# Kernel tuning notes

Hardware: AMD Instinct MI355X
Metric: run time of the kernel (lower is better)

The kernel has to match this reference:

```python
import jax, jax.numpy as jnp
import numpy as np

B, C, H, W = 4, 256, 64, 64
C8 = C // 8


def setup_inputs() -> dict:
    key = jax.random.key(0)
    k1, k2, k3, k4 = jax.random.split(key, 4)
    x = jax.random.normal(k1, (B, C, H, W), dtype=jnp.float32)
    # conv1d(ks=1, bias=False) projections -> plain [out, in] matrices
    Wq = jax.random.normal(k2, (C8, C), dtype=jnp.float32) * (1.0 / np.sqrt(C))
    Wk = jax.random.normal(k3, (C8, C), dtype=jnp.float32) * (1.0 / np.sqrt(C))
    Wv = jax.random.normal(k4, (C, C), dtype=jnp.float32) * (1.0 / np.sqrt(C))
    gamma = jnp.zeros((1,), dtype=jnp.float32)
    return {"x": x, "Wq": Wq, "Wk": Wk, "Wv": Wv, "gamma": gamma}


def reference(x, Wq, Wk, Wv, gamma):
    b, c, h, w = x.shape
    xf = x.reshape(b, c, h * w)                      # [B, C, N]
    f = jnp.einsum('oc,bcn->bon', Wq, xf)            # [B, C/8, N] query
    g = jnp.einsum('oc,bcn->bon', Wk, xf)            # [B, C/8, N] key
    hv = jnp.einsum('oc,bcn->bon', Wv, xf)           # [B, C,   N] value
    # scores[b,i,j] = sum_c f[b,c,i] * g[b,c,j]; softmax over dim=1 (i)
    scores = jnp.einsum('bci,bcj->bij', f, g)        # [B, N, N]
    beta = jax.nn.softmax(scores, axis=1)
    # o[b,c,j] = sum_i hv[b,c,i] * beta[b,i,j]
    o = jnp.einsum('bci,bij->bcj', hv, beta)         # [B, C, N]
    out = gamma[0] * o + xf
    return out.reshape(b, c, h, w)
```

## Files before the change

kernel.cpp:

```cpp
#include <hip/hip_runtime.h>

#define B_  4
#define C_  256
#define C8_ 32
#define N_  4096

#define TJ 128
#define KI 64
#define SPLITS 4

typedef __attribute__((ext_vector_type(8)))  short bf16x8;
typedef __attribute__((ext_vector_type(16))) float f32x16;

union FragAB { bf16x8 v; unsigned short u[8]; };

__device__ __forceinline__ unsigned short f2bf(float x) {
    unsigned u = __float_as_uint(x);
    unsigned r = u + 0x7FFFu + ((u >> 16) & 1u);
    return (unsigned short)(r >> 16);
}
__device__ __forceinline__ unsigned pack2bf(float a, float b) {
    return (unsigned)f2bf(a) | ((unsigned)f2bf(b) << 16);
}

__global__ __launch_bounds__(256) void prep_w_kernel(
    const float* __restrict__ Wq, const float* __restrict__ Wk,
    const float* __restrict__ Wv, unsigned short* __restrict__ Wbf)
{
    int idx = (blockIdx.x * 256 + threadIdx.x) * 4;
    int row = idx >> 8;
    int col = idx & 255;
    const float* src; int r;
    if (row < 32)      { src = Wq; r = row;      }
    else if (row < 64) { src = Wk; r = row - 32; }
    else               { src = Wv; r = row - 64; }
    float4 v = *(const float4*)&src[r * 256 + col];
    uint2 o; o.x = pack2bf(v.x, v.y); o.y = pack2bf(v.z, v.w);
    *(uint2*)&Wbf[idx] = o;
}

__global__ __launch_bounds__(256) void prep_x_kernel(
    const float* __restrict__ x, unsigned short* __restrict__ xT)
{
    __shared__ unsigned short T[64][66];
    int t  = threadIdx.x;
    int b  = blockIdx.z;
    int c0 = blockIdx.y * 64;
    int n0 = blockIdx.x * 64;
    const float* xb = x + (size_t)b * C_ * N_;
    int n_l = t & 63, c_l = t >> 6;
#pragma unroll
    for (int q = 0; q < 16; ++q) {
        int c = c_l * 16 + q;
        T[n_l][c] = f2bf(xb[(size_t)(c0 + c) * N_ + n0 + n_l]);
    }
    __syncthreads();
    unsigned short* xTb = xT + (size_t)b * N_ * C_;
    int c_l2 = t & 63, nb = t >> 6;
#pragma unroll
    for (int q = 0; q < 16; ++q) {
        int n = nb * 16 + q;
        xTb[(size_t)(n0 + n) * C_ + c0 + c_l2] = T[n][c_l2];
    }
}

__global__ __launch_bounds__(256) void proj_mfma_kernel(
    const unsigned short* __restrict__ Wbf, const unsigned short* __restrict__ xT,
    unsigned short* __restrict__ f, unsigned short* __restrict__ g,
    unsigned short* __restrict__ hv)
{
    int t = threadIdx.x, w = t >> 6, lane = t & 63;
    int half = lane >> 5, l31 = lane & 31;
    int b  = blockIdx.y;
    int n0 = blockIdx.x * 32;

    const unsigned short* xb = xT + ((size_t)b * N_ + n0 + l31) * C_;
    int nm = (w < 2) ? 3 : 2;
    int mt0 = w, mt1 = w + 4, mt2 = w + 8;

    f32x16 acc[3];
#pragma unroll
    for (int a = 0; a < 3; ++a) acc[a] = (f32x16)0.f;

#pragma unroll
    for (int ks = 0; ks < 16; ++ks) {
        int kofs = ks * 16 + half * 8;
        bf16x8 bfr = *(const bf16x8*)&xb[kofs];
        bf16x8 a0 = *(const bf16x8*)&Wbf[(size_t)(mt0 * 32 + l31) * 256 + kofs];
        acc[0] = __builtin_amdgcn_mfma_f32_32x32x16_bf16(a0, bfr, acc[0], 0, 0, 0);
        bf16x8 a1 = *(const bf16x8*)&Wbf[(size_t)(mt1 * 32 + l31) * 256 + kofs];
        acc[1] = __builtin_amdgcn_mfma_f32_32x32x16_bf16(a1, bfr, acc[1], 0, 0, 0);
        if (nm == 3) {
            bf16x8 a2 = *(const bf16x8*)&Wbf[(size_t)(mt2 * 32 + l31) * 256 + kofs];
            acc[2] = __builtin_amdgcn_mfma_f32_32x32x16_bf16(a2, bfr, acc[2], 0, 0, 0);
        }
    }

    unsigned short* fb = f  + (size_t)b * C8_ * N_;
    unsigned short* gb = g  + (size_t)b * C8_ * N_;
    unsigned short* hb = hv + (size_t)b * C_  * N_;
#pragma unroll
    for (int im = 0; im < 3; ++im) {
        if (im >= nm) break;
        int mt = (im == 0) ? mt0 : (im == 1) ? mt1 : mt2;
#pragma unroll
        for (int r = 0; r < 16; ++r) {
            int R = mt * 32 + (r & 3) + 8 * (r >> 2) + 4 * half;
            unsigned short v = f2bf(acc[im][r]);
            if (R < 32)       fb[(size_t)R * N_ + n0 + l31] = v;
            else if (R < 64)  gb[(size_t)(R - 64 + 32) * N_ + n0 + l31] = v;
            else              hb[(size_t)(R - 64) * N_ + n0 + l31] = v;
        }
    }
}

__global__ __launch_bounds__(256, 2) void flash_kernel(
    const unsigned short* __restrict__ f, const unsigned short* __restrict__ g,
    const unsigned short* __restrict__ hv, float* __restrict__ o_part,
    float* __restrict__ l_part)
{
    __shared__ unsigned short fT[64][40];
    __shared__ unsigned short hvT[256][72];
    __shared__ unsigned short pT[128][72];

    int t    = threadIdx.x;
    int w    = t >> 6;
    int lane = t & 63;
    int half = lane >> 5;
    int l31  = lane & 31;

    int b  = blockIdx.z;
    int s  = blockIdx.y;
    int j0 = blockIdx.x * TJ;

    const unsigned short* fb = f  + (size_t)b * C8_ * N_;
    const unsigned short* gb = g  + (size_t)b * C8_ * N_;
    const unsigned short* hb = hv + (size_t)b * C_  * N_;

    FragAB gf[2];
#pragma unroll
    for (int ks = 0; ks < 2; ++ks)
#pragma unroll
        for (int r = 0; r < 8; ++r) {
            int ch = ks * 16 + half * 8 + r;
            gf[ks].u[r] = gb[(size_t)ch * N_ + j0 + w * 32 + l31];
        }

    f32x16 acc[8];
#pragma unroll
    for (int a = 0; a < 8; ++a) acc[a] = (f32x16)0.f;
    float lacc = 0.f;

    int i_begin = s * (N_ / SPLITS);
    int i_end   = i_begin + N_ / SPLITS;

    for (int i0 = i_begin; i0 < i_end; i0 += KI) {
        __syncthreads();

        {
            int i   = t & 63;
            int chb = (t >> 6) * 8;
            unsigned short v[8];
#pragma unroll
            for (int q = 0; q < 8; ++q)
                v[q] = fb[(size_t)(chb + q) * N_ + i0 + i];
#pragma unroll
            for (int q = 0; q < 4; ++q)
                *(unsigned*)&fT[i][chb + 2 * q] =
                    (unsigned)v[2 * q] | ((unsigned)v[2 * q + 1] << 16);
        }
        {
            int crow  = t >> 3;
            int chunk = t & 7;
#pragma unroll
            for (int q = 0; q < 8; ++q) {
                int c = crow + 32 * q;
                uint4 v = *(const uint4*)&hb[(size_t)c * N_ + i0 + chunk * 8];
                *(uint4*)&hvT[c][chunk * 8] = v;
            }
        }
        __syncthreads();

#pragma unroll
        for (int it = 0; it < 2; ++it) {
            f32x16 sacc = (f32x16)0.f;
#pragma unroll
            for (int ks = 0; ks < 2; ++ks) {
                bf16x8 af = *(const bf16x8*)&fT[it * 32 + l31][ks * 16 + half * 8];
                sacc = __builtin_amdgcn_mfma_f32_32x32x16_bf16(af, gf[ks].v, sacc, 0, 0, 0);
            }
            float p[16];
#pragma unroll
            for (int r = 0; r < 16; ++r) {
                p[r] = __expf(sacc[r]);
                lacc += p[r];
            }
            int jr = w * 32 + l31;
#pragma unroll
            for (int a = 0; a < 4; ++a) {
                unsigned u0 = pack2bf(p[4 * a + 0], p[4 * a + 1]);
                unsigned u1 = pack2bf(p[4 * a + 2], p[4 * a + 3]);
                uint2 v; v.x = u0; v.y = u1;
                *(uint2*)&pT[jr][it * 32 + 8 * a + 4 * half] = v;
            }
        }
        __syncthreads();

#pragma unroll
        for (int ks4 = 0; ks4 < 4; ++ks4) {
            int kofs = ks4 * 16 + half * 8;
            bf16x8 af[2], bfr[4];
#pragma unroll
            for (int ct = 0; ct < 2; ++ct)
                af[ct] = *(const bf16x8*)&hvT[w * 64 + ct * 32 + l31][kofs];
#pragma unroll
            for (int jt = 0; jt < 4; ++jt)
                bfr[jt] = *(const bf16x8*)&pT[jt * 32 + l31][kofs];
#pragma unroll
            for (int ct = 0; ct < 2; ++ct)
#pragma unroll
                for (int jt = 0; jt < 4; ++jt)
                    acc[ct * 4 + jt] = __builtin_amdgcn_mfma_f32_32x32x16_bf16(
                        af[ct], bfr[jt], acc[ct * 4 + jt], 0, 0, 0);
        }
    }

    float* ob = o_part + (size_t)(b * SPLITS + s) * C_ * N_;
#pragma unroll
    for (int ct = 0; ct < 2; ++ct)
#pragma unroll
        for (int jt = 0; jt < 4; ++jt) {
            f32x16 a = acc[ct * 4 + jt];
#pragma unroll
            for (int r = 0; r < 16; ++r) {
                int c = w * 64 + ct * 32 + (r & 3) + 8 * (r >> 2) + 4 * half;
                int j = j0 + jt * 32 + l31;
                ob[(size_t)c * N_ + j] = a[r];
            }
        }
    float lsum = lacc + __shfl_down(lacc, 32);
    if (lane < 32)
        l_part[(size_t)(b * SPLITS + s) * N_ + j0 + w * 32 + lane] = lsum;
}

__global__ __launch_bounds__(256) void combine_kernel(
    const float* __restrict__ o_part, const float* __restrict__ l_part,
    const float* __restrict__ x, const float* __restrict__ gamma,
    float* __restrict__ out)
{
    int j = blockIdx.x * 256 + threadIdx.x;
    int b = blockIdx.z;
    float l = 0.f;
#pragma unroll
    for (int s = 0; s < SPLITS; ++s)
        l += l_part[(size_t)(b * SPLITS + s) * N_ + j];
    float inv = 1.f / l;
    float gm = gamma[0];
#pragma unroll
    for (int cc = 0; cc < 4; ++cc) {
        int c = blockIdx.y * 4 + cc;
        float o = 0.f;
#pragma unroll
        for (int s = 0; s < SPLITS; ++s)
            o += o_part[((size_t)(b * SPLITS + s) * C_ + c) * N_ + j];
        size_t idx = ((size_t)b * C_ + c) * N_ + j;
        out[idx] = gm * o * inv + x[idx];
    }
}

extern "C" void kernel_launch(void* const* d_in, const int* in_sizes, int n_in,
                              void* d_out, int out_size, void* d_ws, size_t ws_size,
                              hipStream_t stream) {
    const float* x     = (const float*)d_in[0];
    const float* Wq    = (const float*)d_in[1];
    const float* Wk    = (const float*)d_in[2];
    const float* Wv    = (const float*)d_in[3];
    const float* gamma = (const float*)d_in[4];
    float* out = (float*)d_out;

    char* ws = (char*)d_ws;
    float* o_part = (float*)ws;
    float* l_part = o_part + (size_t)SPLITS * B_ * C_ * N_;
    unsigned short* f   = (unsigned short*)(l_part + (size_t)SPLITS * B_ * N_);
    unsigned short* g   = f   + (size_t)B_ * C8_ * N_;
    unsigned short* hv  = g   + (size_t)B_ * C8_ * N_;
    unsigned short* Wbf = hv  + (size_t)B_ * C_  * N_;
    unsigned short* xT  = Wbf + (size_t)(C_ + 2 * C8_) * C_;

    prep_w_kernel<<<dim3(80), 256, 0, stream>>>(Wq, Wk, Wv, Wbf);
    prep_x_kernel<<<dim3(N_ / 64, C_ / 64, B_), 256, 0, stream>>>(x, xT);

    proj_mfma_kernel<<<dim3(N_ / 32, B_), 256, 0, stream>>>(Wbf, xT, f, g, hv);

    flash_kernel<<<dim3(N_ / TJ, SPLITS, B_), 256, 0, stream>>>(f, g, hv, o_part, l_part);

    combine_kernel<<<dim3(N_ / 256, C_ / 4, B_), 256, 0, stream>>>(o_part, l_part, x, gamma, out);
}
```

Baseline: 158.8 us.

## Split flash kernel over channel halves, read operands directly from global, bf16 partials

```diff
diff --git a/kernel.cpp b/kernel.cpp
--- a/kernel.cpp
+++ b/kernel.cpp
@@ -21,6 +21,9 @@
 }
 __device__ __forceinline__ unsigned pack2bf(float a, float b) {
     return (unsigned)f2bf(a) | ((unsigned)f2bf(b) << 16);
+}
+__device__ __forceinline__ float bf2f(unsigned short h) {
+    return __uint_as_float(((unsigned)h) << 16);
 }
 
 __global__ __launch_bounds__(256) void prep_w_kernel(
@@ -66,7 +69,7 @@
 
 __global__ __launch_bounds__(256) void proj_mfma_kernel(
     const unsigned short* __restrict__ Wbf, const unsigned short* __restrict__ xT,
-    unsigned short* __restrict__ f, unsigned short* __restrict__ g,
+    unsigned short* __restrict__ fTg, unsigned short* __restrict__ g,
     unsigned short* __restrict__ hv)
 {
     int t = threadIdx.x, w = t >> 6, lane = t & 63;
@@ -96,7 +99,6 @@
         }
     }
 
-    unsigned short* fb = f  + (size_t)b * C8_ * N_;
     unsigned short* gb = g  + (size_t)b * C8_ * N_;
     unsigned short* hb = hv + (size_t)b * C_  * N_;
 #pragma unroll
@@ -107,21 +109,19 @@
         for (int r = 0; r < 16; ++r) {
             int R = mt * 32 + (r & 3) + 8 * (r >> 2) + 4 * half;
             unsigned short v = f2bf(acc[im][r]);
-            if (R < 32)       fb[(size_t)R * N_ + n0 + l31] = v;
-            else if (R < 64)  gb[(size_t)(R - 64 + 32) * N_ + n0 + l31] = v;
+            if (R < 32)       fTg[((size_t)b * N_ + n0 + l31) * 32 + R] = v;
+            else if (R < 64)  gb[(size_t)(R - 32) * N_ + n0 + l31] = v;
             else              hb[(size_t)(R - 64) * N_ + n0 + l31] = v;
         }
     }
 }
 
-__global__ __launch_bounds__(256, 2) void flash_kernel(
-    const unsigned short* __restrict__ f, const unsigned short* __restrict__ g,
-    const unsigned short* __restrict__ hv, float* __restrict__ o_part,
+__global__ __launch_bounds__(256, 3) void flash_kernel(
+    const unsigned short* __restrict__ fTg, const unsigned short* __restrict__ g,
+    const unsigned short* __restrict__ hv, unsigned short* __restrict__ o_part,
     float* __restrict__ l_part)
 {
-    __shared__ unsigned short fT[64][40];
-    __shared__ unsigned short hvT[256][72];
-    __shared__ unsigned short pT[128][72];
+    __shared__ unsigned short pT[2][128][72];
 
     int t    = threadIdx.x;
     int w    = t >> 6;
@@ -129,13 +129,15 @@
     int half = lane >> 5;
     int l31  = lane & 31;
 
-    int b  = blockIdx.z;
-    int s  = blockIdx.y;
-    int j0 = blockIdx.x * TJ;
-
-    const unsigned short* fb = f  + (size_t)b * C8_ * N_;
-    const unsigned short* gb = g  + (size_t)b * C8_ * N_;
-    const unsigned short* hb = hv + (size_t)b * C_  * N_;
+    int j0    = blockIdx.x * TJ;
+    int chalf = blockIdx.y;
+    int bs    = blockIdx.z;
+    int b     = bs >> 2;
+    int s     = bs & 3;
+
+    const unsigned short* fb = fTg + (size_t)b * N_ * 32;
+    const unsigned short* gb = g   + (size_t)b * C8_ * N_;
+    const unsigned short* hrow = hv + ((size_t)b * C_ + chalf * 128 + w * 32 + l31) * N_;
 
     FragAB gf[2];
 #pragma unroll
@@ -146,47 +148,24 @@
             gf[ks].u[r] = gb[(size_t)ch * N_ + j0 + w * 32 + l31];
         }
 
-    f32x16 acc[8];
-#pragma unroll
-    for (int a = 0; a < 8; ++a) acc[a] = (f32x16)0.f;
+    f32x16 acc[4];
+#pragma unroll
+    for (int a = 0; a < 4; ++a) acc[a] = (f32x16)0.f;
     float lacc = 0.f;
 
     int i_begin = s * (N_ / SPLITS);
-    int i_end   = i_begin + N_ / SPLITS;
-
-    for (int i0 = i_begin; i0 < i_end; i0 += KI) {
-        __syncthreads();
-
-        {
-            int i   = t & 63;
-            int chb = (t >> 6) * 8;
-            unsigned short v[8];
-#pragma unroll
-            for (int q = 0; q < 8; ++q)
-                v[q] = fb[(size_t)(chb + q) * N_ + i0 + i];
-#pragma unroll
-            for (int q = 0; q < 4; ++q)
-                *(unsigned*)&fT[i][chb + 2 * q] =
-                    (unsigned)v[2 * q] | ((unsigned)v[2 * q + 1] << 16);
-        }
-        {
-            int crow  = t >> 3;
-            int chunk = t & 7;
-#pragma unroll
-            for (int q = 0; q < 8; ++q) {
-                int c = crow + 32 * q;
-                uint4 v = *(const uint4*)&hb[(size_t)c * N_ + i0 + chunk * 8];
-                *(uint4*)&hvT[c][chunk * 8] = v;
-            }
-        }
-        __syncthreads();
+
+    for (int ii = 0; ii < (N_ / SPLITS) / KI; ++ii) {
+        int i0  = i_begin + ii * KI;
+        int buf = ii & 1;
 
 #pragma unroll
         for (int it = 0; it < 2; ++it) {
             f32x16 sacc = (f32x16)0.f;
 #pragma unroll
             for (int ks = 0; ks < 2; ++ks) {
-                bf16x8 af = *(const bf16x8*)&fT[it * 32 + l31][ks * 16 + half * 8];
+                bf16x8 af = *(const bf16x8*)&fb[(size_t)(i0 + it * 32 + l31) * 32
+                                                + ks * 16 + half * 8];
                 sacc = __builtin_amdgcn_mfma_f32_32x32x16_bf16(af, gf[ks].v, sacc, 0, 0, 0);
             }
             float p[16];
@@ -198,10 +177,10 @@
             int jr = w * 32 + l31;
 #pragma unroll
             for (int a = 0; a < 4; ++a) {
-                unsigned u0 = pack2bf(p[4 * a + 0], p[4 * a + 1]);
-                unsigned u1 = pack2bf(p[4 * a + 2], p[4 * a + 3]);
-                uint2 v; v.x = u0; v.y = u1;
-                *(uint2*)&pT[jr][it * 32 + 8 * a + 4 * half] = v;
+                uint2 v;
+                v.x = pack2bf(p[4 * a + 0], p[4 * a + 1]);
+                v.y = pack2bf(p[4 * a + 2], p[4 * a + 3]);
+                *(uint2*)&pT[buf][jr][it * 32 + 8 * a + 4 * half] = v;
             }
         }
         __syncthreads();
@@ -209,42 +188,37 @@
 #pragma unroll
         for (int ks4 = 0; ks4 < 4; ++ks4) {
             int kofs = ks4 * 16 + half * 8;
-            bf16x8 af[2], bfr[4];
-#pragma unroll
-            for (int ct = 0; ct < 2; ++ct)
-                af[ct] = *(const bf16x8*)&hvT[w * 64 + ct * 32 + l31][kofs];
+            bf16x8 a = *(const bf16x8*)&hrow[i0 + kofs];
+            bf16x8 bfr[4];
 #pragma unroll
             for (int jt = 0; jt < 4; ++jt)
-                bfr[jt] = *(const bf16x8*)&pT[jt * 32 + l31][kofs];
-#pragma unroll
-            for (int ct = 0; ct < 2; ++ct)
-#pragma unroll
-                for (int jt = 0; jt < 4; ++jt)
-                    acc[ct * 4 + jt] = __builtin_amdgcn_mfma_f32_32x32x16_bf16(
-                        af[ct], bfr[jt], acc[ct * 4 + jt], 0, 0, 0);
-        }
-    }
-
-    float* ob = o_part + (size_t)(b * SPLITS + s) * C_ * N_;
-#pragma unroll
-    for (int ct = 0; ct < 2; ++ct)
-#pragma unroll
-        for (int jt = 0; jt < 4; ++jt) {
-            f32x16 a = acc[ct * 4 + jt];
-#pragma unroll
-            for (int r = 0; r < 16; ++r) {
-                int c = w * 64 + ct * 32 + (r & 3) + 8 * (r >> 2) + 4 * half;
-                int j = j0 + jt * 32 + l31;
-                ob[(size_t)c * N_ + j] = a[r];
-            }
-        }
-    float lsum = lacc + __shfl_down(lacc, 32);
-    if (lane < 32)
-        l_part[(size_t)(b * SPLITS + s) * N_ + j0 + w * 32 + lane] = lsum;
+                bfr[jt] = *(const bf16x8*)&pT[buf][jt * 32 + l31][kofs];
+#pragma unroll
+            for (int jt = 0; jt < 4; ++jt)
+                acc[jt] = __builtin_amdgcn_mfma_f32_32x32x16_bf16(a, bfr[jt], acc[jt], 0, 0, 0);
+        }
+    }
+
+    unsigned short* ob = o_part + (size_t)bs * C_ * N_;
+#pragma unroll
+    for (int jt = 0; jt < 4; ++jt) {
+        f32x16 a = acc[jt];
+#pragma unroll
+        for (int r = 0; r < 16; ++r) {
+            int c = chalf * 128 + w * 32 + (r & 3) + 8 * (r >> 2) + 4 * half;
+            int j = j0 + jt * 32 + l31;
+            ob[(size_t)c * N_ + j] = f2bf(a[r]);
+        }
+    }
+    if (chalf == 0) {
+        float lsum = lacc + __shfl_down(lacc, 32);
+        if (lane < 32)
+            l_part[(size_t)bs * N_ + j0 + w * 32 + lane] = lsum;
+    }
 }
 
 __global__ __launch_bounds__(256) void combine_kernel(
-    const float* __restrict__ o_part, const float* __restrict__ l_part,
+    const unsigned short* __restrict__ o_part, const float* __restrict__ l_part,
     const float* __restrict__ x, const float* __restrict__ gamma,
     float* __restrict__ out)
 {
@@ -262,7 +236,7 @@
         float o = 0.f;
 #pragma unroll
         for (int s = 0; s < SPLITS; ++s)
-            o += o_part[((size_t)(b * SPLITS + s) * C_ + c) * N_ + j];
+            o += bf2f(o_part[((size_t)(b * SPLITS + s) * C_ + c) * N_ + j]);
         size_t idx = ((size_t)b * C_ + c) * N_ + j;
         out[idx] = gm * o * inv + x[idx];
     }
@@ -279,10 +253,10 @@
     float* out = (float*)d_out;
 
     char* ws = (char*)d_ws;
-    float* o_part = (float*)ws;
-    float* l_part = o_part + (size_t)SPLITS * B_ * C_ * N_;
-    unsigned short* f   = (unsigned short*)(l_part + (size_t)SPLITS * B_ * N_);
-    unsigned short* g   = f   + (size_t)B_ * C8_ * N_;
+    unsigned short* o_part = (unsigned short*)ws;
+    float* l_part = (float*)(o_part + (size_t)SPLITS * B_ * C_ * N_);
+    unsigned short* fTg = (unsigned short*)(l_part + (size_t)SPLITS * B_ * N_);
+    unsigned short* g   = fTg + (size_t)B_ * C8_ * N_;
     unsigned short* hv  = g   + (size_t)B_ * C8_ * N_;
     unsigned short* Wbf = hv  + (size_t)B_ * C_  * N_;
     unsigned short* xT  = Wbf + (size_t)(C_ + 2 * C8_) * C_;
@@ -290,9 +264,10 @@
     prep_w_kernel<<<dim3(80), 256, 0, stream>>>(Wq, Wk, Wv, Wbf);
     prep_x_kernel<<<dim3(N_ / 64, C_ / 64, B_), 256, 0, stream>>>(x, xT);
 
-    proj_mfma_kernel<<<dim3(N_ / 32, B_), 256, 0, stream>>>(Wbf, xT, f, g, hv);
-
-    flash_kernel<<<dim3(N_ / TJ, SPLITS, B_), 256, 0, stream>>>(f, g, hv, o_part, l_part);
+    proj_mfma_kernel<<<dim3(N_ / 32, B_), 256, 0, stream>>>(Wbf, xT, fTg, g, hv);
+
+    flash_kernel<<<dim3(N_ / TJ, 2, SPLITS * B_), 256, 0, stream>>>(
+        fTg, g, hv, o_part, l_part);
 
     combine_kernel<<<dim3(N_ / 256, C_ / 4, B_), 256, 0, stream>>>(o_part, l_part, x, gamma, out);
 }
```

Result: slower. 166.1 us (+4.6%).
